# Kernel tuning notes

Hardware: AMD Instinct MI355X
Metric: run time of the kernel (lower is better)

The kernel has to match this reference:

```python
import jax, jax.numpy as jnp
import numpy as np
import math

N_NODES = 20000
N_EDGES = 640000
N_BASIS = 10
NUM_NEIGHBORS = 32.0


def _fctp_scalar_attr(x0, x1, attr, W0, W1):
    """FullyConnectedTensorProduct(irreps_in, '0e' attr) == per-irrep linear
    scaled by the scalar attribute, with e3nn fan-in normalization.
    x0: [N, mul0] scalars, x1: [N, mul1, 3] vectors, attr: [N, 1]."""
    a = attr[:, :1]
    y0 = (x0 * a) @ W0 / jnp.sqrt(jnp.asarray(W0.shape[0], x0.dtype))
    y1 = jnp.einsum('nui,uv->nvi', x1 * a[:, :, None], W1) / jnp.sqrt(jnp.asarray(W1.shape[0], x1.dtype))
    return y0, y1


def setup_inputs() -> dict:
    key = jax.random.key(0)
    ks = jax.random.split(key, 13)
    node_input = jax.random.normal(ks[0], (N_NODES, 80), jnp.float32)
    node_attr = jnp.ones((N_NODES, 1), jnp.float32)
    edge_attr = jax.random.normal(ks[1], (N_EDGES, 4), jnp.float32)
    edge_scalars = jax.random.uniform(ks[2], (N_EDGES, N_BASIS), jnp.float32)
    edge_index = jax.random.randint(ks[3], (2, N_EDGES), 0, N_NODES)
    # learned params
    W_sc0 = jax.random.normal(ks[4], (32, 32), jnp.float32)
    W_sc1 = jax.random.normal(ks[5], (16, 16), jnp.float32)
    W_l1_0 = jax.random.normal(ks[6], (32, 32), jnp.float32)
    W_l1_1 = jax.random.normal(ks[7], (16, 16), jnp.float32)
    W_fc0 = jax.random.normal(ks[8], (N_BASIS, 64), jnp.float32)
    W_fc1 = jax.random.normal(ks[9], (64, 96), jnp.float32)  # 96 = tp.weight_numel
    W_l2_0 = jax.random.normal(ks[10], (48, 32), jnp.float32)
    W_l2_1 = jax.random.normal(ks[11], (48, 16), jnp.float32)
    return dict(node_input=node_input, node_attr=node_attr, edge_attr=edge_attr,
                edge_scalars=edge_scalars, W_sc0=W_sc0, W_sc1=W_sc1,
                W_l1_0=W_l1_0, W_l1_1=W_l1_1, W_fc0=W_fc0, W_fc1=W_fc1,
                W_l2_0=W_l2_0, W_l2_1=W_l2_1, edge_index=edge_index)


def reference(node_input, node_attr, edge_attr, edge_scalars,
              W_sc0, W_sc1, W_l1_0, W_l1_1, W_fc0, W_fc1, W_l2_0, W_l2_1,
              edge_index):
    N = node_input.shape[0]
    x0 = node_input[:, :32]                     # 32x0e
    x1 = node_input[:, 32:].reshape(N, 16, 3)   # 16x1o

    # self-connection and pre-TP linear
    s0, s1 = _fctp_scalar_attr(x0, x1, node_attr, W_sc0, W_sc1)
    y0, y1 = _fctp_scalar_attr(x0, x1, node_attr, W_l1_0, W_l1_1)

    # radial MLP -> per-edge TP weights (e3nn FullyConnectedNet: no bias, fan-in norm, silu)
    h = jax.nn.silu(edge_scalars @ W_fc0 / jnp.sqrt(jnp.asarray(N_BASIS, jnp.float32)))
    w = h @ W_fc1 / jnp.sqrt(jnp.asarray(64.0, jnp.float32))  # [E, 96]
    w_a, w_b, w_c, w_d = w[:, :32], w[:, 32:64], w[:, 64:80], w[:, 80:96]

    src, dst = edge_index[0], edge_index[1]
    xs0 = y0[src]                               # [E, 32]
    xs1 = y1[src]                               # [E, 16, 3]
    e0 = edge_attr[:, :1]                       # [E, 1] 0e sh
    e1 = edge_attr[:, 1:4]                      # [E, 3] 1o sh

    # 'uvu' tensor product paths -> irreps_mid = 32x0e + 16x0e + 32x1o + 16x1o
    m_a = w_a * xs0 * e0                                    # 0e x 0e -> 0e  [E,32]
    m_b = (w_b * xs0)[:, :, None] * e1[:, None, :]          # 0e x 1o -> 1o  [E,32,3]
    m_c = w_c[:, :, None] * xs1 * e0[:, :, None]            # 1o x 0e -> 1o  [E,16,3]
    m_d = w_d * jnp.einsum('eui,ei->eu', xs1, e1) / jnp.sqrt(jnp.asarray(3.0, jnp.float32))  # 1o x 1o -> 0e [E,16]
    mid0 = jnp.concatenate([m_a, m_d], axis=1)              # [E, 48] scalars
    mid1 = jnp.concatenate([m_b, m_c], axis=1)              # [E, 48, 3] vectors

    # scatter-add into destination nodes, normalized by sqrt(num_neighbors)
    inv = 1.0 / jnp.sqrt(jnp.asarray(NUM_NEIGHBORS, jnp.float32))
    agg0 = jax.ops.segment_sum(mid0, dst, num_segments=N) * inv
    agg1 = jax.ops.segment_sum(mid1, dst, num_segments=N) * inv

    # lin2: FCTP(irreps_mid, '0e') -> irreps_out, attr == 1
    z0 = agg0 @ W_l2_0 / jnp.sqrt(jnp.asarray(48.0, jnp.float32))
    z1 = jnp.einsum('nui,uv->nvi', agg1, W_l2_1) / jnp.sqrt(jnp.asarray(48.0, jnp.float32))

    # skip mix: output_mask of sc is all ones here (all out irreps reachable)
    c_s = math.sin(math.pi / 8)
    c_x = math.cos(math.pi / 8)
    out0 = c_s * s0 + c_x * z0
    out1 = c_s * s1 + c_x * z1
    return jnp.concatenate([out0, out1.reshape(N, 48)], axis=1)
```

## Files before the change

### kernel.cpp

```cpp
#include <hip/hip_runtime.h>

#define N_NODES 20000
#define N_EDGES 640000
#define N_MT (N_EDGES/16)

typedef short short8 __attribute__((ext_vector_type(8)));
typedef float f32x4 __attribute__((ext_vector_type(4)));

__device__ __forceinline__ unsigned short f2bf(float x){
  unsigned int u = __builtin_bit_cast(unsigned int, x);
  u += 0x7fffu + ((u >> 16) & 1u);
  return (unsigned short)(u >> 16);
}
__device__ __forceinline__ float bf2f(unsigned short u){
  unsigned int v = ((unsigned int)u) << 16;
  return __builtin_bit_cast(float, v);
}

__device__ __forceinline__ void wave_lds_fence(){
  __asm__ volatile("s_waitcnt lgkmcnt(0)" ::: "memory");
}

#define HIST_BLOCKS ((N_EDGES+255)/256)
#define YN_BLOCKS   (N_NODES/16)
#define AGGZ_BLOCKS 938

__global__ void k_pre(const int* __restrict__ ei, int* __restrict__ counts,
                      const float* __restrict__ ni, const float* __restrict__ na,
                      const float* __restrict__ Wl10, const float* __restrict__ Wl11,
                      unsigned short* __restrict__ y, float4* __restrict__ aggz){
  if (blockIdx.x < HIST_BLOCKS){
    int e = blockIdx.x*256 + threadIdx.x;
    if (e < N_EDGES) atomicAdd(&counts[ei[N_EDGES + e]], 1);
    return;
  }
  if (blockIdx.x >= HIST_BLOCKS + YN_BLOCKS){
    int i = (blockIdx.x - HIST_BLOCKS - YN_BLOCKS)*256 + threadIdx.x;
    if (i < 240000){
      float4 z = {0.f,0.f,0.f,0.f};
      float4* p = aggz + (size_t)i*4;
      p[0]=z; p[1]=z; p[2]=z; p[3]=z;
    }
    return;
  }
  __shared__ float sW0[1024];
  __shared__ float sW1[256];
  __shared__ float sni[16*84];
  __shared__ float sna[16];
  const int t = threadIdx.x;
  const int nb = (blockIdx.x - HIST_BLOCKS)*16;
  for (int i=t; i<1024; i+=256) sW0[i] = Wl10[i];
  if (t < 256) sW1[t] = Wl11[t];
  for (int i=t; i<320; i+=256){
    int n = i/20, q = i - n*20;
    *(float4*)&sni[n*84 + q*4] = *(const float4*)(ni + (size_t)(nb+n)*80 + q*4);
  }
  if (t < 16) sna[t] = na[nb + t];
  __syncthreads();
  for (int i=t; i<1280; i+=256){
    int n = i/80, k = i - n*80;
    const float* row = sni + n*84;
    float a = sna[n];
    float acc = 0.f;
    if (k < 32){
      #pragma unroll
      for (int u=0; u<32; ++u) acc += row[u]*sW0[u*32+k];
      y[(size_t)nb*80 + i] = f2bf(acc * a * 0.17677669529663687f);
    } else {
      int kk = k-32, v = kk/3, ii = kk - v*3;
      #pragma unroll
      for (int u=0; u<16; ++u) acc += row[32+u*3+ii]*sW1[u*16+v];
      y[(size_t)nb*80 + i] = f2bf(acc * a * 0.25f);
    }
  }
}

__global__ void k_alloc(const int* __restrict__ counts, int* __restrict__ ctr,
                        int* __restrict__ cursor){
  __shared__ int wsum[4];
  __shared__ int s_base;
  const int t = threadIdx.x;
  const int lane = t & 63, wv = t >> 6;
  const int n = blockIdx.x*256 + t;
  int v = (n < N_NODES) ? counts[n] : 0;
  int x = v;
  #pragma unroll
  for (int off=1; off<64; off<<=1){
    int sh = __shfl_up(x, off, 64);
    if (lane >= off) x += sh;
  }
  if (lane == 63) wsum[wv] = x;
  __syncthreads();
  if (t == 0){
    int s0 = wsum[0], s1 = wsum[1], s2 = wsum[2], s3 = wsum[3];
    int total = s0 + s1 + s2 + s3;
    wsum[0] = 0; wsum[1] = s0; wsum[2] = s0+s1; wsum[3] = s0+s1+s2;
    s_base = atomicAdd(ctr, total);
  }
  __syncthreads();
  if (n < N_NODES) cursor[n] = s_base + wsum[wv] + (x - v);
}

__global__ void k_fill(const int* __restrict__ ei, const float* __restrict__ ea,
                       const float* __restrict__ es, int* __restrict__ cursor,
                       float4* __restrict__ meta){
  int e = blockIdx.x*256 + threadIdx.x;
  if (e >= N_EDGES) return;
  int s = ei[e], d = ei[N_EDGES + e];
  int pos = atomicAdd(&cursor[d], 1);
  const float* eap = ea + (size_t)e*4;
  const float* esp = es + (size_t)e*10;
  float4 v0, v1, v2, v3;
  v0.x = eap[0]; v0.y = eap[1]; v0.z = eap[2]; v0.w = eap[3];
  v1.x = esp[0]; v1.y = esp[1]; v1.z = esp[2]; v1.w = esp[3];
  v2.x = esp[4]; v2.y = esp[5]; v2.z = esp[6]; v2.w = esp[7];
  v3.x = esp[8]; v3.y = esp[9];
  v3.z = __int_as_float(s); v3.w = __int_as_float(d);
  float4* mp = meta + (size_t)pos*4;
  mp[0] = v0; mp[1] = v1; mp[2] = v2; mp[3] = v3;
}

__global__ __launch_bounds__(256) void k_edge(
    const float4* __restrict__ meta,
    const float* __restrict__ Wfc0, const float* __restrict__ Wfc1,
    const unsigned short* __restrict__ yb, float* __restrict__ agg){
  __shared__ float s_wfc0[640];
  __shared__ unsigned short s_w[4][16*98];
  __shared__ unsigned short s_y[4][16*88];
  __shared__ float s_m[4][16*20];

  const int t = threadIdx.x;
  const int w = t >> 6, l = t & 63;
  const int r = l & 15, part = l >> 4;

  for (int i = t; i < 640; i += 256) s_wfc0[i] = Wfc0[i];

  short8 b0[6], b1[6];
  #pragma unroll
  for (int nt=0; nt<6; ++nt){
    #pragma unroll
    for (int j=0; j<8; ++j){
      b0[nt][j] = (short)f2bf(Wfc1[(     part*8+j)*96 + nt*16 + r]);
      b1[nt][j] = (short)f2bf(Wfc1[(32 + part*8+j)*96 + nt*16 + r]);
    }
  }
  __syncthreads();

  int o_c[3], yo[3], eai[3];
  #pragma unroll
  for (int p=0; p<3; ++p){
    int c = p*64 + l;
    if (c < 32)      { o_c[p]=c;    yo[p]=c;        eai[p]=0; }
    else if (c < 48) { int u=c-32;  o_c[p]=80+u;    yo[p]=32+3*u; eai[p]=0; }
    else if (c < 144){ int idx=c-48;  int u=idx/3, fi=idx-u*3; o_c[p]=32+u; yo[p]=u;        eai[p]=1+fi; }
    else             { int idx=c-144; int u=idx/3, i =idx-u*3; o_c[p]=64+u; yo[p]=32+3*u+i; eai[p]=0; }
  }
  const bool dot0 = (l >= 32) && (l < 48);

  unsigned short* sw = s_w[w];
  unsigned short* sy = s_y[w];
  float* sm = s_m[w];

  const int o0 = (part==0) ? 0 : (part==1) ? 24 : (part==2) ? 40 : 64;
  const bool has3 = (part & 1) == 0;

  const int gw = blockIdx.x*4 + w;
  const int nw = gridDim.x*4;
  const int m0 = (int)(((long long)gw     * N_MT) / nw);
  const int m1 = (int)(((long long)(gw+1) * N_MT) / nw);
  if (m0 >= m1) return;

  float4 mreg = meta[(size_t)m0*64 + l];

  float acc0 = 0.f, acc1 = 0.f, acc2 = 0.f;
  int dcur = -1;

  for (int m = m0; m < m1; ++m){
    const int mnx = (m+1 < m1) ? (m+1) : m;
    float4 mnext = meta[(size_t)mnx*64 + l];

    const int isrc = __float_as_int(__shfl(mreg.z, 4*r + 3));
    const int idst = __float_as_int(__shfl(mreg.w, 4*r + 3));

    {
      const unsigned short* yrow = yb + (size_t)isrc*80;
      uint4 va = *(const uint4*)(yrow + o0);
      uint4 vb = *(const uint4*)(yrow + o0 + 8);
      uint4 vc;
      if (has3) vc = *(const uint4*)(yrow + o0 + 16);
      unsigned short* syr = sy + r*88;
      *(uint4*)(syr + o0)      = va;
      *(uint4*)(syr + o0 + 8)  = vb;
      if (has3) *(uint4*)(syr + o0 + 16) = vc;
    }
    *(float4*)(sm + (l>>2)*20 + (l&3)*4) = mreg;
    wave_lds_fence();

    const float* esr = sm + r*20 + 4;
    float hv0[8], hv1[8];
    #pragma unroll
    for (int j=0; j<8; ++j){ hv0[j]=0.f; hv1[j]=0.f; }
    #pragma unroll
    for (int k=0; k<10; ++k){
      float ev = esr[k];
      const float* wr = s_wfc0 + k*64 + part*8;
      #pragma unroll
      for (int j=0; j<8; ++j){ hv0[j] += ev*wr[j]; hv1[j] += ev*wr[32+j]; }
    }
    short8 a0, a1;
    #pragma unroll
    for (int j=0; j<8; ++j){
      float x0 = hv0[j]*0.31622776601683794f;
      float x1 = hv1[j]*0.31622776601683794f;
      a0[j] = (short)f2bf(x0/(1.f+__expf(-x0)));
      a1[j] = (short)f2bf(x1/(1.f+__expf(-x1)));
    }

    #pragma unroll
    for (int nt=0; nt<6; ++nt){
      f32x4 acc = {0.f,0.f,0.f,0.f};
      acc = __builtin_amdgcn_mfma_f32_16x16x32_bf16(a0, b0[nt], acc, 0,0,0);
      acc = __builtin_amdgcn_mfma_f32_16x16x32_bf16(a1, b1[nt], acc, 0,0,0);
      #pragma unroll
      for (int rr=0; rr<4; ++rr)
        sw[(part*4+rr)*98 + nt*16 + r] = f2bf(acc[rr]*0.125f);
    }
    wave_lds_fence();

    for (int e=0; e<16; ++e){
      int de = __shfl(idst, e);
      if (de != dcur){
        if (dcur >= 0){
          unsafeAtomicAdd(&agg[(size_t)dcur*192 +       l], acc0);
          unsafeAtomicAdd(&agg[(size_t)dcur*192 +  64 + l], acc1);
          unsafeAtomicAdd(&agg[(size_t)dcur*192 + 128 + l], acc2);
        }
        acc0 = acc1 = acc2 = 0.f;
        dcur = de;
      }
      const float* sme = sm + e*20;
      const unsigned short* swe = sw + e*98;
      const unsigned short* sye = sy + e*88;
      float m0v;
      if (dot0){
        m0v = bf2f(swe[o_c[0]]) *
              (bf2f(sye[yo[0]])*sme[1] + bf2f(sye[yo[0]+1])*sme[2] + bf2f(sye[yo[0]+2])*sme[3])
              * 0.5773502691896258f;
      } else {
        m0v = bf2f(swe[o_c[0]]) * bf2f(sye[yo[0]]) * sme[eai[0]];
      }
      acc0 += m0v;
      acc1 += bf2f(swe[o_c[1]]) * bf2f(sye[yo[1]]) * sme[eai[1]];
      acc2 += bf2f(swe[o_c[2]]) * bf2f(sye[yo[2]]) * sme[eai[2]];
    }
    wave_lds_fence();

    mreg = mnext;
  }
  if (dcur >= 0){
    unsafeAtomicAdd(&agg[(size_t)dcur*192 +       l], acc0);
    unsafeAtomicAdd(&agg[(size_t)dcur*192 +  64 + l], acc1);
    unsafeAtomicAdd(&agg[(size_t)dcur*192 + 128 + l], acc2);
  }
}

__global__ void k_finish(const float* __restrict__ ni, const float* __restrict__ na,
    const float* __restrict__ Wsc0, const float* __restrict__ Wsc1,
    const float* __restrict__ Wl20, const float* __restrict__ Wl21,
    const float* __restrict__ agg, float* __restrict__ out){
  __shared__ float sWsc0[1024];
  __shared__ float sWsc1[256];
  __shared__ float sWl20[1536];
  __shared__ float sWl21[768];
  __shared__ float sni[16*84];
  __shared__ float sag[16*196];
  __shared__ float sna[16];
  const int t = threadIdx.x;
  const int nb = blockIdx.x*16;
  for (int i=t; i<1024; i+=256) sWsc0[i] = Wsc0[i];
  if (t < 256) sWsc1[t] = Wsc1[t];
  for (int i=t; i<1536; i+=256) sWl20[i] = Wl20[i];
  for (int i=t; i<768;  i+=256) sWl21[i] = Wl21[i];
  for (int i=t; i<320;  i+=256){
    int n = i/20, q = i - n*20;
    *(float4*)&sni[n*84 + q*4] = *(const float4*)(ni + (size_t)(nb+n)*80 + q*4);
  }
  for (int i=t; i<768;  i+=256){
    int n = i/48, q = i - n*48;
    *(float4*)&sag[n*196 + q*4] = *(const float4*)(agg + (size_t)(nb+n)*192 + q*4);
  }
  if (t < 16) sna[t] = na[nb + t];
  __syncthreads();

  const float c_s = 0.3826834323650898f;
  const float c_x = 0.9238795325112867f;
  const float zscale = 0.17677669529663687f * 0.14433756729740643f;
  for (int i=t; i<1280; i+=256){
    int n = i/80, k = i - n*80;
    const float* row = sni + n*84;
    const float* ag  = sag + n*196;
    float a = sna[n];
    float s = 0.f, z = 0.f;
    if (k < 32){
      #pragma unroll
      for (int u=0; u<32; ++u) s += row[u]*sWsc0[u*32+k];
      s *= a * 0.17677669529663687f;
      #pragma unroll
      for (int u=0; u<48; ++u) z += ag[u]*sWl20[u*32+k];
    } else {
      int kk=k-32, v=kk/3, ii=kk-v*3;
      #pragma unroll
      for (int u=0; u<16; ++u) s += row[32+u*3+ii]*sWsc1[u*16+v];
      s *= a * 0.25f;
      #pragma unroll
      for (int u=0; u<48; ++u) z += ag[48+u*3+ii]*sWl21[u*16+v];
    }
    out[(size_t)nb*80 + i] = c_s*s + c_x*z*zscale;
  }
}

extern "C" void kernel_launch(void* const* d_in, const int* in_sizes, int n_in,
                              void* d_out, int out_size, void* d_ws, size_t ws_size,
                              hipStream_t stream){
  const float* node_input   = (const float*)d_in[0];
  const float* node_attr    = (const float*)d_in[1];
  const float* edge_attr    = (const float*)d_in[2];
  const float* edge_scalars = (const float*)d_in[3];
  const float* W_sc0 = (const float*)d_in[4];
  const float* W_sc1 = (const float*)d_in[5];
  const float* W_l1_0 = (const float*)d_in[6];
  const float* W_l1_1 = (const float*)d_in[7];
  const float* W_fc0 = (const float*)d_in[8];
  const float* W_fc1 = (const float*)d_in[9];
  const float* W_l2_0 = (const float*)d_in[10];
  const float* W_l2_1 = (const float*)d_in[11];
  const int* edge_index = (const int*)d_in[12];
  float* out = (float*)d_out;

  char* ws = (char*)d_ws;
  unsigned short* y = (unsigned short*)ws;
  float*  agg    = (float*)(ws + 3200000);
  int*    counts = (int*)(ws + 18560000);
  int*    ctr    = (int*)(ws + 18640000);
  int*    cursor = (int*)(ws + 18640064);
  float4* meta   = (float4*)(ws + 18722048);

  hipMemsetAsync(counts, 0, 80064, stream);

  k_pre  <<<HIST_BLOCKS + YN_BLOCKS + AGGZ_BLOCKS, 256, 0, stream>>>(
            edge_index, counts, node_input, node_attr, W_l1_0, W_l1_1,
            y, (float4*)agg);
  k_alloc<<<(N_NODES+255)/256, 256, 0, stream>>>(counts, ctr, cursor);
  k_fill <<<(N_EDGES+255)/256, 256, 0, stream>>>(edge_index, edge_attr, edge_scalars,
                                                 cursor, meta);
  k_edge <<<1280, 256, 0, stream>>>(meta, W_fc0, W_fc1, y, agg);
  k_finish<<<YN_BLOCKS, 256, 0, stream>>>(node_input, node_attr, W_sc0, W_sc1,
                                          W_l2_0, W_l2_1, agg, out);
}
```

Baseline: 349.5 us.

## Pack per-edge metadata into bf16 and 16-bit indices, vectorize histogram loads

Per-edge metadata (edge scalars, edge attributes, src/dst indices) is stored as bf16 values plus 16-bit packed indices, shrinking each record from 64 to 32 bytes. The edge kernel now reads uint2 per lane and unpacks into the same LDS layout. This halves metadata write and read traffic between the fill and edge kernels, at the cost of bf16 rounding on edge attributes and scalars and a 16-bit node index limit, which only holds because N_NODES is below 65536. The histogram pass also loads four destination indices per thread with one int4 read.

```diff
diff --git a/kernel.cpp b/kernel.cpp
--- a/kernel.cpp
+++ b/kernel.cpp
@@ -7,21 +7,27 @@
 typedef short short8 __attribute__((ext_vector_type(8)));
 typedef float f32x4 __attribute__((ext_vector_type(4)));
 
-__device__ __forceinline__ unsigned short f2bf(float x){
+__device__ __forceinline__ unsigned int f2bf(float x){
   unsigned int u = __builtin_bit_cast(unsigned int, x);
   u += 0x7fffu + ((u >> 16) & 1u);
-  return (unsigned short)(u >> 16);
+  return u >> 16;
 }
 __device__ __forceinline__ float bf2f(unsigned short u){
   unsigned int v = ((unsigned int)u) << 16;
   return __builtin_bit_cast(float, v);
 }
+__device__ __forceinline__ float bflo(unsigned int u){
+  return __builtin_bit_cast(float, u << 16);
+}
+__device__ __forceinline__ float bfhi(unsigned int u){
+  return __builtin_bit_cast(float, u & 0xffff0000u);
+}
 
 __device__ __forceinline__ void wave_lds_fence(){
   __asm__ volatile("s_waitcnt lgkmcnt(0)" ::: "memory");
 }
 
-#define HIST_BLOCKS ((N_EDGES+255)/256)
+#define HIST_BLOCKS 625
 #define YN_BLOCKS   (N_NODES/16)
 #define AGGZ_BLOCKS 938
 
@@ -30,8 +36,14 @@
                       const float* __restrict__ Wl10, const float* __restrict__ Wl11,
                       unsigned short* __restrict__ y, float4* __restrict__ aggz){
   if (blockIdx.x < HIST_BLOCKS){
-    int e = blockIdx.x*256 + threadIdx.x;
-    if (e < N_EDGES) atomicAdd(&counts[ei[N_EDGES + e]], 1);
+    int i = blockIdx.x*256 + threadIdx.x;
+    if (i < N_EDGES/4){
+      int4 d4 = *(const int4*)(ei + N_EDGES + i*4);
+      atomicAdd(&counts[d4.x], 1);
+      atomicAdd(&counts[d4.y], 1);
+      atomicAdd(&counts[d4.z], 1);
+      atomicAdd(&counts[d4.w], 1);
+    }
     return;
   }
   if (blockIdx.x >= HIST_BLOCKS + YN_BLOCKS){
@@ -65,12 +77,12 @@
     if (k < 32){
       #pragma unroll
       for (int u=0; u<32; ++u) acc += row[u]*sW0[u*32+k];
-      y[(size_t)nb*80 + i] = f2bf(acc * a * 0.17677669529663687f);
+      y[(size_t)nb*80 + i] = (unsigned short)f2bf(acc * a * 0.17677669529663687f);
     } else {
       int kk = k-32, v = kk/3, ii = kk - v*3;
       #pragma unroll
       for (int u=0; u<16; ++u) acc += row[32+u*3+ii]*sW1[u*16+v];
-      y[(size_t)nb*80 + i] = f2bf(acc * a * 0.25f);
+      y[(size_t)nb*80 + i] = (unsigned short)f2bf(acc * a * 0.25f);
     }
   }
 }
@@ -103,25 +115,28 @@
 
 __global__ void k_fill(const int* __restrict__ ei, const float* __restrict__ ea,
                        const float* __restrict__ es, int* __restrict__ cursor,
-                       float4* __restrict__ meta){
+                       uint4* __restrict__ meta){
   int e = blockIdx.x*256 + threadIdx.x;
   if (e >= N_EDGES) return;
   int s = ei[e], d = ei[N_EDGES + e];
   int pos = atomicAdd(&cursor[d], 1);
   const float* eap = ea + (size_t)e*4;
   const float* esp = es + (size_t)e*10;
-  float4 v0, v1, v2, v3;
-  v0.x = eap[0]; v0.y = eap[1]; v0.z = eap[2]; v0.w = eap[3];
-  v1.x = esp[0]; v1.y = esp[1]; v1.z = esp[2]; v1.w = esp[3];
-  v2.x = esp[4]; v2.y = esp[5]; v2.z = esp[6]; v2.w = esp[7];
-  v3.x = esp[8]; v3.y = esp[9];
-  v3.z = __int_as_float(s); v3.w = __int_as_float(d);
-  float4* mp = meta + (size_t)pos*4;
-  mp[0] = v0; mp[1] = v1; mp[2] = v2; mp[3] = v3;
+  unsigned int u0 = f2bf(esp[0]) | (f2bf(esp[1])<<16);
+  unsigned int u1 = f2bf(esp[2]) | (f2bf(esp[3])<<16);
+  unsigned int u2 = f2bf(esp[4]) | (f2bf(esp[5])<<16);
+  unsigned int u3 = f2bf(esp[6]) | (f2bf(esp[7])<<16);
+  unsigned int u4 = f2bf(esp[8]) | (f2bf(esp[9])<<16);
+  unsigned int u5 = f2bf(eap[0]) | (f2bf(eap[1])<<16);
+  unsigned int u6 = f2bf(eap[2]) | (f2bf(eap[3])<<16);
+  unsigned int u7 = ((unsigned int)s << 16) | (unsigned int)d;
+  uint4* mp = meta + (size_t)pos*2;
+  mp[0] = make_uint4(u0,u1,u2,u3);
+  mp[1] = make_uint4(u4,u5,u6,u7);
 }
 
 __global__ __launch_bounds__(256) void k_edge(
-    const float4* __restrict__ meta,
+    const uint2* __restrict__ meta,
     const float* __restrict__ Wfc0, const float* __restrict__ Wfc1,
     const unsigned short* __restrict__ yb, float* __restrict__ agg){
   __shared__ float s_wfc0[640];
@@ -132,6 +147,7 @@
   const int t = threadIdx.x;
   const int w = t >> 6, l = t & 63;
   const int r = l & 15, part = l >> 4;
+  const int q = l & 3;
 
   for (int i = t; i < 640; i += 256) s_wfc0[i] = Wfc0[i];
 
@@ -170,17 +186,18 @@
   const int m1 = (int)(((long long)(gw+1) * N_MT) / nw);
   if (m0 >= m1) return;
 
-  float4 mreg = meta[(size_t)m0*64 + l];
+  uint2 mreg = meta[(size_t)m0*64 + l];
 
   float acc0 = 0.f, acc1 = 0.f, acc2 = 0.f;
   int dcur = -1;
 
   for (int m = m0; m < m1; ++m){
     const int mnx = (m+1 < m1) ? (m+1) : m;
-    float4 mnext = meta[(size_t)mnx*64 + l];
-
-    const int isrc = __float_as_int(__shfl(mreg.z, 4*r + 3));
-    const int idst = __float_as_int(__shfl(mreg.w, 4*r + 3));
+    uint2 mnext = meta[(size_t)mnx*64 + l];
+
+    const int packed = __shfl((int)mreg.y, 4*r + 3);
+    const int isrc = ((unsigned int)packed) >> 16;
+    const int idst = packed & 0xffff;
 
     {
       const unsigned short* yrow = yb + (size_t)isrc*80;
@@ -193,7 +210,20 @@
       *(uint4*)(syr + o0 + 8)  = vb;
       if (has3) *(uint4*)(syr + o0 + 16) = vc;
     }
-    *(float4*)(sm + (l>>2)*20 + (l&3)*4) = mreg;
+    {
+      float* sme = sm + (l>>2)*20;
+      float f0 = bflo(mreg.x), f1 = bfhi(mreg.x);
+      float f2 = bflo(mreg.y), f3 = bfhi(mreg.y);
+      if (q == 0){
+        sme[4]=f0; sme[5]=f1; sme[6]=f2; sme[7]=f3;
+      } else if (q == 1){
+        sme[8]=f0; sme[9]=f1; sme[10]=f2; sme[11]=f3;
+      } else if (q == 2){
+        sme[12]=f0; sme[13]=f1; sme[0]=f2; sme[1]=f3;
+      } else {
+        sme[2]=f0; sme[3]=f1;
+      }
+    }
     wave_lds_fence();
 
     const float* esr = sm + r*20 + 4;
@@ -223,7 +253,7 @@
       acc = __builtin_amdgcn_mfma_f32_16x16x32_bf16(a1, b1[nt], acc, 0,0,0);
       #pragma unroll
       for (int rr=0; rr<4; ++rr)
-        sw[(part*4+rr)*98 + nt*16 + r] = f2bf(acc[rr]*0.125f);
+        sw[(part*4+rr)*98 + nt*16 + r] = (unsigned short)f2bf(acc[rr]*0.125f);
     }
     wave_lds_fence();
 
@@ -343,7 +373,7 @@
   int*    counts = (int*)(ws + 18560000);
   int*    ctr    = (int*)(ws + 18640000);
   int*    cursor = (int*)(ws + 18640064);
-  float4* meta   = (float4*)(ws + 18722048);
+  uint4*  meta   = (uint4*)(ws + 18722048);
 
   hipMemsetAsync(counts, 0, 80064, stream);
 
@@ -353,7 +383,7 @@
   k_alloc<<<(N_NODES+255)/256, 256, 0, stream>>>(counts, ctr, cursor);
   k_fill <<<(N_EDGES+255)/256, 256, 0, stream>>>(edge_index, edge_attr, edge_scalars,
                                                  cursor, meta);
-  k_edge <<<1280, 256, 0, stream>>>(meta, W_fc0, W_fc1, y, agg);
+  k_edge <<<1280, 256, 0, stream>>>((const uint2*)meta, W_fc0, W_fc1, y, agg);
   k_finish<<<YN_BLOCKS, 256, 0, stream>>>(node_input, node_attr, W_sc0, W_sc1,
                                           W_l2_0, W_l2_1, agg, out);
 }
```

After: 337.4 us. 3.5% less time.
